# Kernel tuning notes

Measured on AMD Instinct MI355X. Metric: run time of the kernel, lower is better.

## Reference

```python
import jax, jax.numpy as jnp
import numpy as np

B, L, O, K, H = 8192, 128, 512, 8, 20  # batch, num_latent, num_obs, causes/node, hidden


def setup_inputs() -> dict:
    key = jax.random.key(0)
    ks = jax.random.split(key, 7)
    x = jax.random.normal(ks[0], (B, L), dtype=jnp.float32)
    # noise ~ Normal(0, 0.1), one scalar per (sample, observed node); noise_coeff = 1.0
    noise = 0.1 * jax.random.normal(ks[1], (B, O), dtype=jnp.float32)
    # latent-cause indices per observed node (fixed in-degree K)
    cause_idx = jax.random.randint(ks[2], (O, K), 0, L, dtype=jnp.int32)
    # per-node MLP weights: Linear(K+1,H) -> tanh -> Linear(H,H) -> tanh -> Linear(H,1)
    W1 = jax.random.normal(ks[3], (O, K + 1, H), dtype=jnp.float32) / np.sqrt(K + 1).astype(np.float32)
    b1 = jnp.zeros((O, H), dtype=jnp.float32)
    W2 = jax.random.normal(ks[4], (O, H, H), dtype=jnp.float32) / np.sqrt(H).astype(np.float32)
    b2 = jnp.zeros((O, H), dtype=jnp.float32)
    W3 = jax.random.normal(ks[5], (O, H), dtype=jnp.float32) / np.sqrt(H).astype(np.float32)
    b3 = jnp.zeros((O,), dtype=jnp.float32)
    return {"x": x, "noise": noise, "cause_idx": cause_idx,
            "W1": W1, "b1": b1, "W2": W2, "b2": b2, "W3": W3, "b3": b3}


def reference(x, noise, cause_idx, W1, b1, W2, b2, W3, b3):
    # Gather each observed node's latent causes: [B, O, K]
    gathered = x[:, cause_idx]
    # Prepend the noise column (torch.cat((noise, x_subset), axis=1)): [B, O, K+1]
    inp = jnp.concatenate([noise[..., None], gathered], axis=-1)
    # Per-node tiny MLP as grouped batched GEMMs
    h = jnp.tanh(jnp.einsum('boi,oih->boh', inp, W1) + b1)   # [B, O, H]
    h = jnp.tanh(jnp.einsum('boh,ohg->bog', h, W2) + b2)     # [B, O, H]
    out = jnp.einsum('boh,oh->bo', h, W3) + b3               # [B, O] (concat of per-node outputs)
    return out
```

## Files before the change

### kernel.cpp

```cpp
#include <hip/hip_runtime.h>

#define B_TOT 8192
#define O_DIM 512
#define L_DIM 128
#define K_DIM 8
#define H_DIM 20

#define TB 64
#define G  16
#define NW 4
#define NTH 256
#define XSTR 65
#define NSTR 17

__device__ __forceinline__ float fast_tanh(float x) {
    float e = __builtin_amdgcn_exp2f(x * 2.885390081777927f);
    float r = __builtin_amdgcn_rcpf(1.0f + e);
    return 1.0f - 2.0f * r;
}

__global__ __launch_bounds__(NTH, 4) void medil_fused(
    const float* __restrict__ x, const float* __restrict__ noise,
    const int* __restrict__ cause_idx,
    const float* __restrict__ W1, const float* __restrict__ b1,
    const float* __restrict__ W2, const float* __restrict__ b2,
    const float* __restrict__ W3, const float* __restrict__ b3,
    float* __restrict__ out)
{
    __shared__ float xT[L_DIM * XSTR];
    __shared__ float nt[TB * NSTR];

    const int tid = threadIdx.x;
    const int o0 = (blockIdx.x & 31) * G;
    const int b0 = (blockIdx.x >> 5) * TB;

    {
        const float4* xg = (const float4*)(x + (size_t)b0 * L_DIM);
        #pragma unroll
        for (int i = 0; i < 8; ++i) {
            int idx = tid + NTH * i;
            int r = idx >> 5, c4 = idx & 31;
            float4 v = xg[r * 32 + c4];
            xT[(c4 * 4 + 0) * XSTR + r] = v.x;
            xT[(c4 * 4 + 1) * XSTR + r] = v.y;
            xT[(c4 * 4 + 2) * XSTR + r] = v.z;
            xT[(c4 * 4 + 3) * XSTR + r] = v.w;
        }
    }
    {
        int r = tid >> 2, c4 = tid & 3;
        float4 v = *(const float4*)(noise + (size_t)(b0 + r) * O_DIM + o0 + c4 * 4);
        nt[r * NSTR + c4 * 4 + 0] = v.x;
        nt[r * NSTR + c4 * 4 + 1] = v.y;
        nt[r * NSTR + c4 * 4 + 2] = v.z;
        nt[r * NSTR + c4 * 4 + 3] = v.w;
    }
    __syncthreads();

    const int lane = tid & 63;
    const int wv = tid >> 6;

    #pragma unroll
    for (int it = 0; it < G / NW; ++it) {
        const int ol = __builtin_amdgcn_readfirstlane(wv * (G / NW) + it);
        const int o  = o0 + ol;

        const float* w1p = W1 + (size_t)o * (K_DIM + 1) * H_DIM;
        const float* b1p = b1 + (size_t)o * H_DIM;
        const float* w2p = W2 + (size_t)o * H_DIM * H_DIM;
        const float* b2p = b2 + (size_t)o * H_DIM;
        const float* w3p = W3 + (size_t)o * H_DIM;
        const int*   cip = cause_idx + (size_t)o * K_DIM;

        float xi[K_DIM];
        #pragma unroll
        for (int k = 0; k < K_DIM; ++k)
            xi[k] = xT[cip[k] * XSTR + lane];
        float inp0 = nt[lane * NSTR + ol];

        float a1[H_DIM];
        #pragma unroll
        for (int h = 0; h < H_DIM; ++h)
            a1[h] = fmaf(inp0, w1p[h], b1p[h]);
        #pragma unroll
        for (int k = 0; k < K_DIM; ++k)
            #pragma unroll
            for (int h = 0; h < H_DIM; ++h)
                a1[h] = fmaf(xi[k], w1p[(k + 1) * H_DIM + h], a1[h]);
        #pragma unroll
        for (int h = 0; h < H_DIM; ++h) a1[h] = fast_tanh(a1[h]);

        float a2[H_DIM];
        #pragma unroll
        for (int g = 0; g < H_DIM; ++g) a2[g] = b2p[g];
        #pragma unroll
        for (int h = 0; h < H_DIM; ++h)
            #pragma unroll
            for (int g = 0; g < H_DIM; ++g)
                a2[g] = fmaf(a1[h], w2p[h * H_DIM + g], a2[g]);
        #pragma unroll
        for (int g = 0; g < H_DIM; ++g) a2[g] = fast_tanh(a2[g]);

        float r = b3[o];
        #pragma unroll
        for (int h = 0; h < H_DIM; ++h) r = fmaf(a2[h], w3p[h], r);
        out[(size_t)(b0 + lane) * O_DIM + o] = r;
    }
}

extern "C" void kernel_launch(void* const* d_in, const int* in_sizes, int n_in,
                              void* d_out, int out_size, void* d_ws, size_t ws_size,
                              hipStream_t stream) {
    const float* x         = (const float*)d_in[0];
    const float* noise     = (const float*)d_in[1];
    const int*   cause_idx = (const int*)d_in[2];
    const float* W1        = (const float*)d_in[3];
    const float* b1        = (const float*)d_in[4];
    const float* W2        = (const float*)d_in[5];
    const float* b2        = (const float*)d_in[6];
    const float* W3        = (const float*)d_in[7];
    const float* b3        = (const float*)d_in[8];
    float* out = (float*)d_out;

    dim3 grid((B_TOT / TB) * (O_DIM / G));
    dim3 block(NTH);
    hipLaunchKernelGGL(medil_fused, grid, block, 0, stream,
                       x, noise, cause_idx, W1, b1, W2, b2, W3, b3, out);
}
```

Baseline: 190.2 us.

## Use packed fp16 dot2 for per-node MLP with prepacked weight layout

Adds a pre-pass kernel that repacks each node's weights into a contiguous struct with fp16 pairs. The main kernel stores the transposed x tile in fp16 LDS and does layers 1–3 with v_dot2 (fp16 products accumulated in fp32), which halves the FMA count and shrinks the LDS footprint so occupancy can go up (launch bounds 7). It costs an extra kernel launch every call and reduces precision of activations and weights to fp16. The fp32 path is kept as a fallback when the workspace is too small.

```diff
diff --git a/kernel.cpp b/kernel.cpp
--- a/kernel.cpp
+++ b/kernel.cpp
@@ -13,13 +13,179 @@
 #define XSTR 65
 #define NSTR 17
 
+typedef _Float16 h2 __attribute__((ext_vector_type(2)));
+
 __device__ __forceinline__ float fast_tanh(float x) {
     float e = __builtin_amdgcn_exp2f(x * 2.885390081777927f);
     float r = __builtin_amdgcn_rcpf(1.0f + e);
     return 1.0f - 2.0f * r;
 }
 
-__global__ __launch_bounds__(NTH, 4) void medil_fused(
+__device__ __forceinline__ float dot2(h2 a, h2 b, float c) {
+#if __has_builtin(__builtin_amdgcn_fdot2)
+    return __builtin_amdgcn_fdot2(a, b, c, false);
+#else
+    return fmaf((float)a[0], (float)b[0], fmaf((float)a[1], (float)b[1], c));
+#endif
+}
+
+__device__ __forceinline__ h2 uh2(unsigned u) {
+    union { unsigned u; h2 h; } c; c.u = u; return c.h;
+}
+
+__device__ __forceinline__ h2 pkrtz(float a, float b) {
+    auto t = __builtin_amdgcn_cvt_pkrtz(a, b);
+    return __builtin_bit_cast(h2, t);
+}
+
+__device__ __forceinline__ unsigned pk_rn(float a, float b) {
+    unsigned short ua = __builtin_bit_cast(unsigned short, (_Float16)a);
+    unsigned short ub = __builtin_bit_cast(unsigned short, (_Float16)b);
+    return (unsigned)ua | ((unsigned)ub << 16);
+}
+
+struct __align__(16) PackedW {
+    float    b1[H_DIM];
+    float    w1n[H_DIM];
+    unsigned w1pk[4][H_DIM];
+    unsigned w2pk[H_DIM][10];
+    float    b2[H_DIM];
+    unsigned w3pk[10];
+    float    b3;
+    float    pad;
+};
+
+__global__ __launch_bounds__(64) void pack_weights(
+    const float* __restrict__ W1, const float* __restrict__ b1,
+    const float* __restrict__ W2, const float* __restrict__ b2,
+    const float* __restrict__ W3, const float* __restrict__ b3,
+    PackedW* __restrict__ pw)
+{
+    const int o = blockIdx.x;
+    const int t = threadIdx.x;
+    PackedW* p = pw + o;
+    const float* w1 = W1 + (size_t)o * (K_DIM + 1) * H_DIM;
+    const float* w2 = W2 + (size_t)o * H_DIM * H_DIM;
+    if (t < H_DIM) {
+        p->b1[t]  = b1[o * H_DIM + t];
+        p->w1n[t] = w1[t];
+        p->b2[t]  = b2[o * H_DIM + t];
+    }
+    for (int i = t; i < 4 * H_DIM; i += 64) {
+        int kp = i / H_DIM, h = i % H_DIM;
+        p->w1pk[kp][h] = pk_rn(w1[(2 * kp + 1) * H_DIM + h],
+                               w1[(2 * kp + 2) * H_DIM + h]);
+    }
+    for (int i = t; i < H_DIM * 10; i += 64) {
+        int g = i / 10, hp = i % 10;
+        p->w2pk[g][hp] = pk_rn(w2[(2 * hp) * H_DIM + g],
+                               w2[(2 * hp + 1) * H_DIM + g]);
+    }
+    if (t < 10) p->w3pk[t] = pk_rn(W3[o * H_DIM + 2 * t], W3[o * H_DIM + 2 * t + 1]);
+    if (t == 0) { p->b3 = b3[o]; p->pad = 0.f; }
+}
+
+__global__ __launch_bounds__(NTH, 7) void medil_fused_f16(
+    const float* __restrict__ x, const float* __restrict__ noise,
+    const int* __restrict__ cause_idx, const PackedW* __restrict__ pw,
+    float* __restrict__ out)
+{
+    __shared__ _Float16 xT[L_DIM * XSTR];
+    __shared__ float    nt[TB * NSTR];
+
+    const int tid = threadIdx.x;
+    const int o0 = (blockIdx.x & 31) * G;
+    const int b0 = (blockIdx.x >> 5) * TB;
+
+    {
+        const float4* xg = (const float4*)(x + (size_t)b0 * L_DIM);
+        #pragma unroll
+        for (int i = 0; i < 8; ++i) {
+            int idx = tid + NTH * i;
+            int r = idx >> 5, c4 = idx & 31;
+            float4 v = xg[r * 32 + c4];
+            xT[(c4 * 4 + 0) * XSTR + r] = (_Float16)v.x;
+            xT[(c4 * 4 + 1) * XSTR + r] = (_Float16)v.y;
+            xT[(c4 * 4 + 2) * XSTR + r] = (_Float16)v.z;
+            xT[(c4 * 4 + 3) * XSTR + r] = (_Float16)v.w;
+        }
+    }
+    {
+        int r = tid >> 2, c4 = tid & 3;
+        float4 v = *(const float4*)(noise + (size_t)(b0 + r) * O_DIM + o0 + c4 * 4);
+        nt[r * NSTR + c4 * 4 + 0] = v.x;
+        nt[r * NSTR + c4 * 4 + 1] = v.y;
+        nt[r * NSTR + c4 * 4 + 2] = v.z;
+        nt[r * NSTR + c4 * 4 + 3] = v.w;
+    }
+    __syncthreads();
+
+    const int lane = tid & 63;
+    const int wv = tid >> 6;
+
+    #pragma unroll
+    for (int it = 0; it < G / NW; ++it) {
+        const int ol = __builtin_amdgcn_readfirstlane(wv * (G / NW) + it);
+        const int o  = o0 + ol;
+
+        const PackedW* P = pw + o;
+        const int* cip = cause_idx + (size_t)o * K_DIM;
+
+        _Float16 xi[K_DIM];
+        #pragma unroll
+        for (int k = 0; k < K_DIM; ++k)
+            xi[k] = xT[cip[k] * XSTR + lane];
+        h2 xp[4];
+        #pragma unroll
+        for (int kp = 0; kp < 4; ++kp) {
+            h2 t; t[0] = xi[2 * kp]; t[1] = xi[2 * kp + 1];
+            xp[kp] = t;
+        }
+        float inp0 = nt[lane * NSTR + ol];
+
+        float a1[H_DIM];
+        #pragma unroll
+        for (int h = 0; h < H_DIM; ++h)
+            a1[h] = fmaf(inp0, P->w1n[h], P->b1[h]);
+        #pragma unroll
+        for (int kp = 0; kp < 4; ++kp)
+            #pragma unroll
+            for (int h = 0; h < H_DIM; ++h)
+                a1[h] = dot2(xp[kp], uh2(P->w1pk[kp][h]), a1[h]);
+        #pragma unroll
+        for (int h = 0; h < H_DIM; ++h) a1[h] = fast_tanh(a1[h]);
+
+        h2 ap[10];
+        #pragma unroll
+        for (int hp = 0; hp < 10; ++hp)
+            ap[hp] = pkrtz(a1[2 * hp], a1[2 * hp + 1]);
+
+        float a2[H_DIM];
+        #pragma unroll
+        for (int g = 0; g < H_DIM; ++g) {
+            float acc = P->b2[g];
+            #pragma unroll
+            for (int hp = 0; hp < 10; ++hp)
+                acc = dot2(ap[hp], uh2(P->w2pk[g][hp]), acc);
+            a2[g] = acc;
+        }
+        #pragma unroll
+        for (int g = 0; g < H_DIM; ++g) a2[g] = fast_tanh(a2[g]);
+
+        h2 tp[10];
+        #pragma unroll
+        for (int hp = 0; hp < 10; ++hp)
+            tp[hp] = pkrtz(a2[2 * hp], a2[2 * hp + 1]);
+        float r = P->b3;
+        #pragma unroll
+        for (int hp = 0; hp < 10; ++hp)
+            r = dot2(tp[hp], uh2(P->w3pk[hp]), r);
+        out[(size_t)(b0 + lane) * O_DIM + o] = r;
+    }
+}
+
+#define XSTRF 65
+__global__ __launch_bounds__(NTH, 4) void medil_fused_legacy(
     const float* __restrict__ x, const float* __restrict__ noise,
     const int* __restrict__ cause_idx,
     const float* __restrict__ W1, const float* __restrict__ b1,
@@ -27,7 +193,7 @@
     const float* __restrict__ W3, const float* __restrict__ b3,
     float* __restrict__ out)
 {
-    __shared__ float xT[L_DIM * XSTR];
+    __shared__ float xT[L_DIM * XSTRF];
     __shared__ float nt[TB * NSTR];
 
     const int tid = threadIdx.x;
@@ -41,10 +207,10 @@
             int idx = tid + NTH * i;
             int r = idx >> 5, c4 = idx & 31;
             float4 v = xg[r * 32 + c4];
-            xT[(c4 * 4 + 0) * XSTR + r] = v.x;
-            xT[(c4 * 4 + 1) * XSTR + r] = v.y;
-            xT[(c4 * 4 + 2) * XSTR + r] = v.z;
-            xT[(c4 * 4 + 3) * XSTR + r] = v.w;
+            xT[(c4 * 4 + 0) * XSTRF + r] = v.x;
+            xT[(c4 * 4 + 1) * XSTRF + r] = v.y;
+            xT[(c4 * 4 + 2) * XSTRF + r] = v.z;
+            xT[(c4 * 4 + 3) * XSTRF + r] = v.w;
         }
     }
     {
@@ -75,7 +241,7 @@
         float xi[K_DIM];
         #pragma unroll
         for (int k = 0; k < K_DIM; ++k)
-            xi[k] = xT[cip[k] * XSTR + lane];
+            xi[k] = xT[cip[k] * XSTRF + lane];
         float inp0 = nt[lane * NSTR + ol];
 
         float a1[H_DIM];
@@ -124,6 +290,15 @@
 
     dim3 grid((B_TOT / TB) * (O_DIM / G));
     dim3 block(NTH);
-    hipLaunchKernelGGL(medil_fused, grid, block, 0, stream,
-                       x, noise, cause_idx, W1, b1, W2, b2, W3, b3, out);
-}
+
+    if (ws_size >= sizeof(PackedW) * O_DIM) {
+        PackedW* pw = (PackedW*)d_ws;
+        hipLaunchKernelGGL(pack_weights, dim3(O_DIM), dim3(64), 0, stream,
+                           W1, b1, W2, b2, W3, b3, pw);
+        hipLaunchKernelGGL(medil_fused_f16, grid, block, 0, stream,
+                           x, noise, cause_idx, pw, out);
+    } else {
+        hipLaunchKernelGGL(medil_fused_legacy, grid, block, 0, stream,
+                           x, noise, cause_idx, W1, b1, W2, b2, W3, b3, out);
+    }
+}
```

New measurement: 165.0 us, median of 2. -13.3%, faster.
